# Kernel tuning notes

Measured on AMD Instinct MI355X. Metric: run time of the kernel, lower is better.

Reference implementation:

```python
import jax, jax.numpy as jnp
import numpy as np

TOP_K = 2
NUM_EXPERTS = 64
AUX_COEF = 0.01


def setup_inputs() -> dict:
    key = jax.random.key(0)
    kx, kw = jax.random.split(key)
    B, S, D, E = 4, 4096, 2048, NUM_EXPERTS
    x = jax.random.normal(kx, (B, S, D), dtype=jnp.float32)
    # nn.Linear default init ~ U(-1/sqrt(D), 1/sqrt(D))
    W = jax.random.uniform(kw, (E, D), dtype=jnp.float32,
                           minval=-1.0 / np.sqrt(D), maxval=1.0 / np.sqrt(D))
    return {"x": x, "W": W}


def reference(x, W):
    B, S, D = x.shape
    E = W.shape[0]
    # router projection (no bias)
    logits = jnp.einsum('bsd,ed->bse', x, W)          # [B,S,E]
    probs = jax.nn.softmax(logits, axis=-1)           # [B,S,E]
    top_k_gates, top_k_indices = jax.lax.top_k(probs, TOP_K)  # [B,S,K]
    top_k_gates = top_k_gates / (jnp.sum(top_k_gates, axis=-1, keepdims=True) + 1e-9)
    # aux loss: fraction of routed slots per expert (one-hot mean) x mean router prob
    total_slots = B * S * TOP_K
    counts = jnp.zeros((E,), dtype=jnp.float32).at[top_k_indices.reshape(-1)].add(1.0)
    avg_tokens_per_expert = counts / total_slots      # == one_hot(idx).mean(dims 0,1,2)
    avg_router_prob = jnp.mean(probs, axis=(0, 1))    # [E]
    aux_loss = AUX_COEF * E * jnp.sum(avg_tokens_per_expert * avg_router_prob)
    return top_k_indices, top_k_gates, aux_loss
```

## Files before the change

### kernel.cpp

```cpp
#include <hip/hip_runtime.h>
#include <math.h>

#define NTOK 16384
#define DDIM 2048
#define NEXP 64
#define TM   32
#define NBLK (NTOK / TM)
#define NCH  32
#define NS   64

typedef _Float16 half4v __attribute__((ext_vector_type(4)));
typedef _Float16 half8v __attribute__((ext_vector_type(8)));
typedef float    f32x4  __attribute__((ext_vector_type(4)));

__global__ __launch_bounds__(256) void prep_kernel(const float* __restrict__ W,
                                                   _Float16* __restrict__ Wh,
                                                   _Float16* __restrict__ Wl,
                                                   float* __restrict__ accg) {
    int idx = blockIdx.x * 256 + threadIdx.x;
    int e = idx >> 11, k = idx & 2047;
    float w = W[idx];
    _Float16 h = (_Float16)w;
    _Float16 l = (_Float16)(w - (float)h);
    int S = k >> 5, nb = e >> 4, nl = e & 15, q = (k >> 3) & 3, j = k & 7;
    size_t off = (size_t)S * 2048 + nb * 512 + q * 128 + nl * 8 + j;
    Wh[off] = h;
    Wl[off] = l;
    if (blockIdx.x == 0 && threadIdx.x < 128) accg[threadIdx.x] = 0.0f;
}

__device__ inline void cvt_store(_Float16* __restrict__ Hp, _Float16* __restrict__ Lp,
                                 int off, float4 v) {
    half4v h, l;
    h.x = (_Float16)v.x; l.x = (_Float16)(v.x - (float)h.x);
    h.y = (_Float16)v.y; l.y = (_Float16)(v.y - (float)h.y);
    h.z = (_Float16)v.z; l.z = (_Float16)(v.z - (float)h.z);
    h.w = (_Float16)v.w; l.w = (_Float16)(v.w - (float)h.w);
    *(half4v*)&Hp[off] = h;
    *(half4v*)&Lp[off] = l;
}

#define MFMA16(a, b, c) __builtin_amdgcn_mfma_f32_16x16x32_f16((a), (b), (c), 0, 0, 0)

__global__ __launch_bounds__(256) void router_kernel(
    const float* __restrict__ x, const _Float16* __restrict__ Wh,
    const _Float16* __restrict__ Wl, float* __restrict__ accg,
    float* __restrict__ out)
{
    __shared__ __align__(16) _Float16 Ah[2][2048];
    __shared__ __align__(16) _Float16 Al[2][2048];
    __shared__ float lgt[TM][NEXP + 1];
    __shared__ float cnt[NEXP];

    const int tid  = threadIdx.x;
    const int lane = tid & 63;
    const int wv   = __builtin_amdgcn_readfirstlane(tid >> 6);
    const int m0   = blockIdx.x * TM;

    if (tid < NEXP) cnt[tid] = 0.0f;

    const int tok0 = tid >> 4;
    const int kk0  = (tid & 15) * 4;
    const int s0   = kk0 >> 5, q0 = (kk0 >> 3) & 3, j00 = kk0 & 7;
    const int offA0 = (s0 * 64 + q0 * 16 + tok0) * 8 + j00;
    const int offA1 = offA0 + 1024;

    const float* gx0 = x + (size_t)(m0 + tok0) * DDIM + kk0;
    const float* gx1 = gx0 + (size_t)16 * DDIM;

    const _Float16* Whp = Wh + wv * 512 + lane * 8;
    const _Float16* Wlp = Wl + wv * 512 + lane * 8;

    f32x4 acc0 = {0.f, 0.f, 0.f, 0.f};
    f32x4 acc1 = {0.f, 0.f, 0.f, 0.f};

    float4 stg[2][2];
    stg[0][0] = *(const float4*)(gx0);
    stg[0][1] = *(const float4*)(gx1);
    stg[1][0] = *(const float4*)(gx0 + 64);
    stg[1][1] = *(const float4*)(gx1 + 64);
    half8v whC = *(const half8v*)(Whp);
    half8v wlC = *(const half8v*)(Wlp);

    for (int ch = 0; ch < NCH; ++ch) {
        const int p = ch & 1;
        cvt_store(&Ah[p][0], &Al[p][0], offA0, stg[p][0]);
        cvt_store(&Ah[p][0], &Al[p][0], offA1, stg[p][1]);
        const int cf = (ch + 2 < NCH) ? ch + 2 : 0;
        stg[p][0] = *(const float4*)(gx0 + cf * 64);
        stg[p][1] = *(const float4*)(gx1 + cf * 64);
        __syncthreads();
        #pragma unroll
        for (int s = 0; s < 2; ++s) {
            const int Sg  = ch * 2 + s;
            const int SgN = (Sg + 1) & (NS - 1);
            half8v whN = *(const half8v*)(Whp + (size_t)SgN * 2048);
            half8v wlN = *(const half8v*)(Wlp + (size_t)SgN * 2048);
            half8v a0h = *(const half8v*)&Ah[p][(s * 64 + lane) * 8];
            half8v a0l = *(const half8v*)&Al[p][(s * 64 + lane) * 8];
            half8v a1h = *(const half8v*)&Ah[p][((2 + s) * 64 + lane) * 8];
            half8v a1l = *(const half8v*)&Al[p][((2 + s) * 64 + lane) * 8];
            acc0 = MFMA16(a0l, wlC, acc0);
            acc0 = MFMA16(a0l, whC, acc0);
            acc0 = MFMA16(a0h, wlC, acc0);
            acc0 = MFMA16(a0h, whC, acc0);
            acc1 = MFMA16(a1l, wlC, acc1);
            acc1 = MFMA16(a1l, whC, acc1);
            acc1 = MFMA16(a1h, wlC, acc1);
            acc1 = MFMA16(a1h, whC, acc1);
            whC = whN;
            wlC = wlN;
        }
    }

    {
        const int q  = lane >> 4;
        const int nl = lane & 15;
        #pragma unroll
        for (int r = 0; r < 4; ++r) {
            lgt[q * 4 + r][wv * 16 + nl]      = acc0[r];
            lgt[16 + q * 4 + r][wv * 16 + nl] = acc1[r];
        }
    }
    __syncthreads();

    const int m = tid >> 3;
    const int j = tid & 7;
    float l[8];
    #pragma unroll
    for (int i = 0; i < 8; ++i) l[i] = lgt[m][j * 8 + i];

    float mx = l[0];
    #pragma unroll
    for (int i = 1; i < 8; ++i) mx = fmaxf(mx, l[i]);
    #pragma unroll
    for (int off = 1; off < 8; off <<= 1) mx = fmaxf(mx, __shfl_xor(mx, off, 8));

    float ev[8];
    float zs = 0.f;
    float v1 = -INFINITY, v2 = -INFINITY;
    int i1 = 0, i2 = 0;
    #pragma unroll
    for (int i = 0; i < 8; ++i) {
        ev[i] = __expf(l[i] - mx);
        zs += ev[i];
        int e = j * 8 + i;
        if (l[i] > v1)      { v2 = v1; i2 = i1; v1 = l[i]; i1 = e; }
        else if (l[i] > v2) { v2 = l[i]; i2 = e; }
    }
    #pragma unroll
    for (int off = 1; off < 8; off <<= 1) zs += __shfl_xor(zs, off, 8);

    #pragma unroll
    for (int off = 1; off < 8; off <<= 1) {
        float ov1 = __shfl_xor(v1, off, 8);
        int   oi1 = __shfl_xor(i1, off, 8);
        float ov2 = __shfl_xor(v2, off, 8);
        int   oi2 = __shfl_xor(i2, off, 8);
        bool afirst = (v1 > ov1) || (v1 == ov1 && i1 < oi1);
        if (afirst) {
            bool t = (v2 > ov1) || (v2 == ov1 && i2 < oi1);
            v2 = t ? v2 : ov1;
            i2 = t ? i2 : oi1;
        } else {
            bool t = (ov2 > v1) || (ov2 == v1 && oi2 < i1);
            v2 = t ? ov2 : v1;
            i2 = t ? oi2 : i1;
            v1 = ov1;
            i1 = oi1;
        }
    }

    const float invz = 1.0f / zs;
    if (j == 0) {
        float p1 = invz;
        float p2 = __expf(v2 - mx) * invz;
        float sden = p1 + p2 + 1e-9f;
        int tok = m0 + m;
        out[tok * 2 + 0] = (float)i1;
        out[tok * 2 + 1] = (float)i2;
        out[32768 + tok * 2 + 0] = p1 / sden;
        out[32768 + tok * 2 + 1] = p2 / sden;
        atomicAdd(&cnt[i1], 1.0f);
        atomicAdd(&cnt[i2], 1.0f);
    }

    #pragma unroll
    for (int i = 0; i < 8; ++i) lgt[m][j * 8 + i] = ev[i] * invz;
    __syncthreads();

    if (tid < NEXP) {
        atomicAdd(&accg[tid], cnt[tid]);
    } else if (tid < 128) {
        int e = tid - 64;
        float s = 0.f;
        #pragma unroll 8
        for (int t = 0; t < TM; ++t) s += lgt[t][e];
        atomicAdd(&accg[64 + e], s);
    }
}

__global__ void finalize_kernel(const float* __restrict__ accg,
                                float* __restrict__ out)
{
    int t = threadIdx.x;
    float c = accg[t];
    float p = accg[64 + t];
    float term = (c / (float)(NTOK * 2)) * (p / (float)NTOK);
    #pragma unroll
    for (int off = 1; off < 64; off <<= 1) term += __shfl_xor(term, off, 64);
    if (t == 0) out[65536] = 0.01f * (float)NEXP * term;
}

extern "C" void kernel_launch(void* const* d_in, const int* in_sizes, int n_in,
                              void* d_out, int out_size, void* d_ws, size_t ws_size,
                              hipStream_t stream) {
    const float* x = (const float*)d_in[0];
    const float* W = (const float*)d_in[1];
    float* out  = (float*)d_out;
    float* accg = (float*)d_ws;
    _Float16* Wh = (_Float16*)(accg + 128);
    _Float16* Wl = Wh + (size_t)DDIM * NEXP;

    prep_kernel<<<512, 256, 0, stream>>>(W, Wh, Wl, accg);
    router_kernel<<<NBLK, 256, 0, stream>>>(x, Wh, Wl, accg, out);
    finalize_kernel<<<1, 64, 0, stream>>>(accg, out);
}
```

Measured before the change: 241.9 us.

## Load x fragments directly into registers and drop LDS staging and lo*lo MFMA

Each wave now loads its own x rows straight from global memory into MFMA operand layout and converts them to hi/lo fp16 in registers. This removes the shared-memory staging buffers and the per-chunk __syncthreads. A register prefetch ring runs four k-steps ahead for x and two ahead for W. The lo*lo MFMA term is dropped, going from four to three MFMAs per product. The cost is that every one of the four waves redundantly loads and converts the same 32 token rows, which raises global/L2 traffic and register pressure, and precision drops slightly.

```diff
diff --git a/kernel.cpp b/kernel.cpp
--- a/kernel.cpp
+++ b/kernel.cpp
@@ -6,12 +6,12 @@
 #define NEXP 64
 #define TM   32
 #define NBLK (NTOK / TM)
-#define NCH  32
 #define NS   64
 
-typedef _Float16 half4v __attribute__((ext_vector_type(4)));
 typedef _Float16 half8v __attribute__((ext_vector_type(8)));
 typedef float    f32x4  __attribute__((ext_vector_type(4)));
+
+#define MFMA16(a, b, c) __builtin_amdgcn_mfma_f32_16x16x32_f16((a), (b), (c), 0, 0, 0)
 
 __global__ __launch_bounds__(256) void prep_kernel(const float* __restrict__ W,
                                                    _Float16* __restrict__ Wh,
@@ -29,26 +29,21 @@
     if (blockIdx.x == 0 && threadIdx.x < 128) accg[threadIdx.x] = 0.0f;
 }
 
-__device__ inline void cvt_store(_Float16* __restrict__ Hp, _Float16* __restrict__ Lp,
-                                 int off, float4 v) {
-    half4v h, l;
-    h.x = (_Float16)v.x; l.x = (_Float16)(v.x - (float)h.x);
-    h.y = (_Float16)v.y; l.y = (_Float16)(v.y - (float)h.y);
-    h.z = (_Float16)v.z; l.z = (_Float16)(v.z - (float)h.z);
-    h.w = (_Float16)v.w; l.w = (_Float16)(v.w - (float)h.w);
-    *(half4v*)&Hp[off] = h;
-    *(half4v*)&Lp[off] = l;
-}
-
-#define MFMA16(a, b, c) __builtin_amdgcn_mfma_f32_16x16x32_f16((a), (b), (c), 0, 0, 0)
+__device__ inline void cvt8(const float4* f, half8v& h, half8v& l) {
+    const float* p = (const float*)f;
+    #pragma unroll
+    for (int i = 0; i < 8; ++i) {
+        _Float16 hi = (_Float16)p[i];
+        h[i] = hi;
+        l[i] = (_Float16)(p[i] - (float)hi);
+    }
+}
 
 __global__ __launch_bounds__(256) void router_kernel(
     const float* __restrict__ x, const _Float16* __restrict__ Wh,
     const _Float16* __restrict__ Wl, float* __restrict__ accg,
     float* __restrict__ out)
 {
-    __shared__ __align__(16) _Float16 Ah[2][2048];
-    __shared__ __align__(16) _Float16 Al[2][2048];
     __shared__ float lgt[TM][NEXP + 1];
     __shared__ float cnt[NEXP];
 
@@ -59,57 +54,55 @@
 
     if (tid < NEXP) cnt[tid] = 0.0f;
 
-    const int tok0 = tid >> 4;
-    const int kk0  = (tid & 15) * 4;
-    const int s0   = kk0 >> 5, q0 = (kk0 >> 3) & 3, j00 = kk0 & 7;
-    const int offA0 = (s0 * 64 + q0 * 16 + tok0) * 8 + j00;
-    const int offA1 = offA0 + 1024;
-
-    const float* gx0 = x + (size_t)(m0 + tok0) * DDIM + kk0;
-    const float* gx1 = gx0 + (size_t)16 * DDIM;
-
-    const _Float16* Whp = Wh + wv * 512 + lane * 8;
-    const _Float16* Wlp = Wl + wv * 512 + lane * 8;
+    const int mrow = lane & 15;
+    const int kg   = (lane >> 4) * 8;
+    const float* ax0 = x + (size_t)(m0 + mrow) * DDIM + kg;
+    const float* ax1 = ax0 + (size_t)16 * DDIM;
+
+    const _Float16* whp = Wh + wv * 512 + lane * 8;
+    const _Float16* wlp = Wl + wv * 512 + lane * 8;
 
     f32x4 acc0 = {0.f, 0.f, 0.f, 0.f};
     f32x4 acc1 = {0.f, 0.f, 0.f, 0.f};
 
-    float4 stg[2][2];
-    stg[0][0] = *(const float4*)(gx0);
-    stg[0][1] = *(const float4*)(gx1);
-    stg[1][0] = *(const float4*)(gx0 + 64);
-    stg[1][1] = *(const float4*)(gx1 + 64);
-    half8v whC = *(const half8v*)(Whp);
-    half8v wlC = *(const half8v*)(Wlp);
-
-    for (int ch = 0; ch < NCH; ++ch) {
-        const int p = ch & 1;
-        cvt_store(&Ah[p][0], &Al[p][0], offA0, stg[p][0]);
-        cvt_store(&Ah[p][0], &Al[p][0], offA1, stg[p][1]);
-        const int cf = (ch + 2 < NCH) ? ch + 2 : 0;
-        stg[p][0] = *(const float4*)(gx0 + cf * 64);
-        stg[p][1] = *(const float4*)(gx1 + cf * 64);
-        __syncthreads();
+    float4 fa[4][2][2];
+    half8v wbh[2], wbl[2];
+
+    #pragma unroll
+    for (int s = 0; s < 4; ++s) {
+        fa[s][0][0] = *(const float4*)(ax0 + s * 32);
+        fa[s][0][1] = *(const float4*)(ax0 + s * 32 + 4);
+        fa[s][1][0] = *(const float4*)(ax1 + s * 32);
+        fa[s][1][1] = *(const float4*)(ax1 + s * 32 + 4);
+    }
+    #pragma unroll
+    for (int s = 0; s < 2; ++s) {
+        wbh[s] = *(const half8v*)(whp + (size_t)s * 2048);
+        wbl[s] = *(const half8v*)(wlp + (size_t)s * 2048);
+    }
+
+    for (int mc = 0; mc < NS / 4; ++mc) {
         #pragma unroll
-        for (int s = 0; s < 2; ++s) {
-            const int Sg  = ch * 2 + s;
-            const int SgN = (Sg + 1) & (NS - 1);
-            half8v whN = *(const half8v*)(Whp + (size_t)SgN * 2048);
-            half8v wlN = *(const half8v*)(Wlp + (size_t)SgN * 2048);
-            half8v a0h = *(const half8v*)&Ah[p][(s * 64 + lane) * 8];
-            half8v a0l = *(const half8v*)&Al[p][(s * 64 + lane) * 8];
-            half8v a1h = *(const half8v*)&Ah[p][((2 + s) * 64 + lane) * 8];
-            half8v a1l = *(const half8v*)&Al[p][((2 + s) * 64 + lane) * 8];
-            acc0 = MFMA16(a0l, wlC, acc0);
-            acc0 = MFMA16(a0l, whC, acc0);
-            acc0 = MFMA16(a0h, wlC, acc0);
-            acc0 = MFMA16(a0h, whC, acc0);
-            acc1 = MFMA16(a1l, wlC, acc1);
-            acc1 = MFMA16(a1l, whC, acc1);
-            acc1 = MFMA16(a1h, wlC, acc1);
-            acc1 = MFMA16(a1h, whC, acc1);
-            whC = whN;
-            wlC = wlN;
+        for (int sub = 0; sub < 4; ++sub) {
+            const int s = mc * 4 + sub;
+            half8v a0h, a0l, a1h, a1l;
+            cvt8(fa[sub][0], a0h, a0l);
+            cvt8(fa[sub][1], a1h, a1l);
+            half8v bh = wbh[sub & 1], bl = wbl[sub & 1];
+            const int sa = (s + 4) & (NS - 1);
+            fa[sub][0][0] = *(const float4*)(ax0 + sa * 32);
+            fa[sub][0][1] = *(const float4*)(ax0 + sa * 32 + 4);
+            fa[sub][1][0] = *(const float4*)(ax1 + sa * 32);
+            fa[sub][1][1] = *(const float4*)(ax1 + sa * 32 + 4);
+            const int sw = (s + 2) & (NS - 1);
+            wbh[sub & 1] = *(const half8v*)(whp + (size_t)sw * 2048);
+            wbl[sub & 1] = *(const half8v*)(wlp + (size_t)sw * 2048);
+            acc0 = MFMA16(a0l, bh, acc0);
+            acc0 = MFMA16(a0h, bl, acc0);
+            acc0 = MFMA16(a0h, bh, acc0);
+            acc1 = MFMA16(a1l, bh, acc1);
+            acc1 = MFMA16(a1h, bl, acc1);
+            acc1 = MFMA16(a1h, bh, acc1);
         }
     }
 
```

Result: slower. 362.2 us (+49.7%).

## Halve router token tile to 16 and drop low-low MFMA term

Applied to the files above, without the earlier changes.

Reduces tokens per block from 32 to 16, doubling the grid to 1024 blocks and halving LDS use per block, with one MFMA accumulator per wave. Drops the lo*lo product of the split-fp16 GEMM (3 MFMAs instead of 4 per step). Prefetches W two slices ahead with a two-entry register ring instead of one ahead. Re-reads W from L2 twice as often per token and slightly lowers logit precision, which may affect top-k ties.

```diff
diff --git a/kernel.cpp b/kernel.cpp
--- a/kernel.cpp
+++ b/kernel.cpp
@@ -4,7 +4,7 @@
 #define NTOK 16384
 #define DDIM 2048
 #define NEXP 64
-#define TM   32
+#define TM   16
 #define NBLK (NTOK / TM)
 #define NCH  32
 #define NS   64
@@ -12,6 +12,8 @@
 typedef _Float16 half4v __attribute__((ext_vector_type(4)));
 typedef _Float16 half8v __attribute__((ext_vector_type(8)));
 typedef float    f32x4  __attribute__((ext_vector_type(4)));
+
+#define MFMA16(a, b, c) __builtin_amdgcn_mfma_f32_16x16x32_f16((a), (b), (c), 0, 0, 0)
 
 __global__ __launch_bounds__(256) void prep_kernel(const float* __restrict__ W,
                                                    _Float16* __restrict__ Wh,
@@ -40,15 +42,13 @@
     *(half4v*)&Lp[off] = l;
 }
 
-#define MFMA16(a, b, c) __builtin_amdgcn_mfma_f32_16x16x32_f16((a), (b), (c), 0, 0, 0)
-
 __global__ __launch_bounds__(256) void router_kernel(
     const float* __restrict__ x, const _Float16* __restrict__ Wh,
     const _Float16* __restrict__ Wl, float* __restrict__ accg,
     float* __restrict__ out)
 {
-    __shared__ __align__(16) _Float16 Ah[2][2048];
-    __shared__ __align__(16) _Float16 Al[2][2048];
+    __shared__ __align__(16) _Float16 Ah[2][1024];
+    __shared__ __align__(16) _Float16 Al[2][1024];
     __shared__ float lgt[TM][NEXP + 1];
     __shared__ float cnt[NEXP];
 
@@ -62,54 +62,43 @@
     const int tok0 = tid >> 4;
     const int kk0  = (tid & 15) * 4;
     const int s0   = kk0 >> 5, q0 = (kk0 >> 3) & 3, j00 = kk0 & 7;
-    const int offA0 = (s0 * 64 + q0 * 16 + tok0) * 8 + j00;
-    const int offA1 = offA0 + 1024;
-
-    const float* gx0 = x + (size_t)(m0 + tok0) * DDIM + kk0;
-    const float* gx1 = gx0 + (size_t)16 * DDIM;
-
-    const _Float16* Whp = Wh + wv * 512 + lane * 8;
-    const _Float16* Wlp = Wl + wv * 512 + lane * 8;
-
-    f32x4 acc0 = {0.f, 0.f, 0.f, 0.f};
-    f32x4 acc1 = {0.f, 0.f, 0.f, 0.f};
-
-    float4 stg[2][2];
-    stg[0][0] = *(const float4*)(gx0);
-    stg[0][1] = *(const float4*)(gx1);
-    stg[1][0] = *(const float4*)(gx0 + 64);
-    stg[1][1] = *(const float4*)(gx1 + 64);
-    half8v whC = *(const half8v*)(Whp);
-    half8v wlC = *(const half8v*)(Wlp);
+    const int offA = (s0 * 64 + q0 * 16 + tok0) * 8 + j00;
+
+    const float* gx = x + (size_t)(m0 + tok0) * DDIM + kk0;
+
+    const _Float16* whp = Wh + wv * 512 + lane * 8;
+    const _Float16* wlp = Wl + wv * 512 + lane * 8;
+
+    f32x4 acc = {0.f, 0.f, 0.f, 0.f};
+
+    float4 stg[2];
+    stg[0] = *(const float4*)(gx);
+    stg[1] = *(const float4*)(gx + 64);
+    half8v wbh[2], wbl[2];
+    #pragma unroll
+    for (int s = 0; s < 2; ++s) {
+        wbh[s] = *(const half8v*)(whp + (size_t)s * 2048);
+        wbl[s] = *(const half8v*)(wlp + (size_t)s * 2048);
+    }
 
     for (int ch = 0; ch < NCH; ++ch) {
         const int p = ch & 1;
-        cvt_store(&Ah[p][0], &Al[p][0], offA0, stg[p][0]);
-        cvt_store(&Ah[p][0], &Al[p][0], offA1, stg[p][1]);
+        cvt_store(&Ah[p][0], &Al[p][0], offA, stg[p]);
         const int cf = (ch + 2 < NCH) ? ch + 2 : 0;
-        stg[p][0] = *(const float4*)(gx0 + cf * 64);
-        stg[p][1] = *(const float4*)(gx1 + cf * 64);
+        stg[p] = *(const float4*)(gx + cf * 64);
         __syncthreads();
         #pragma unroll
         for (int s = 0; s < 2; ++s) {
             const int Sg  = ch * 2 + s;
-            const int SgN = (Sg + 1) & (NS - 1);
-            half8v whN = *(const half8v*)(Whp + (size_t)SgN * 2048);
-            half8v wlN = *(const half8v*)(Wlp + (size_t)SgN * 2048);
-            half8v a0h = *(const half8v*)&Ah[p][(s * 64 + lane) * 8];
-            half8v a0l = *(const half8v*)&Al[p][(s * 64 + lane) * 8];
-            half8v a1h = *(const half8v*)&Ah[p][((2 + s) * 64 + lane) * 8];
-            half8v a1l = *(const half8v*)&Al[p][((2 + s) * 64 + lane) * 8];
-            acc0 = MFMA16(a0l, wlC, acc0);
-            acc0 = MFMA16(a0l, whC, acc0);
-            acc0 = MFMA16(a0h, wlC, acc0);
-            acc0 = MFMA16(a0h, whC, acc0);
-            acc1 = MFMA16(a1l, wlC, acc1);
-            acc1 = MFMA16(a1l, whC, acc1);
-            acc1 = MFMA16(a1h, wlC, acc1);
-            acc1 = MFMA16(a1h, whC, acc1);
-            whC = whN;
-            wlC = wlN;
+            const int SgN = (Sg + 2) & (NS - 1);
+            half8v ah = *(const half8v*)&Ah[p][(s * 64 + lane) * 8];
+            half8v al = *(const half8v*)&Al[p][(s * 64 + lane) * 8];
+            half8v bh = wbh[s], bl = wbl[s];
+            wbh[s] = *(const half8v*)(whp + (size_t)SgN * 2048);
+            wbl[s] = *(const half8v*)(wlp + (size_t)SgN * 2048);
+            acc = MFMA16(al, bh, acc);
+            acc = MFMA16(ah, bl, acc);
+            acc = MFMA16(ah, bh, acc);
         }
     }
 
@@ -117,76 +106,76 @@
         const int q  = lane >> 4;
         const int nl = lane & 15;
         #pragma unroll
-        for (int r = 0; r < 4; ++r) {
-            lgt[q * 4 + r][wv * 16 + nl]      = acc0[r];
-            lgt[16 + q * 4 + r][wv * 16 + nl] = acc1[r];
-        }
+        for (int r = 0; r < 4; ++r)
+            lgt[q * 4 + r][wv * 16 + nl] = acc[r];
     }
     __syncthreads();
 
-    const int m = tid >> 3;
-    const int j = tid & 7;
-    float l[8];
-    #pragma unroll
-    for (int i = 0; i < 8; ++i) l[i] = lgt[m][j * 8 + i];
-
-    float mx = l[0];
-    #pragma unroll
-    for (int i = 1; i < 8; ++i) mx = fmaxf(mx, l[i]);
-    #pragma unroll
-    for (int off = 1; off < 8; off <<= 1) mx = fmaxf(mx, __shfl_xor(mx, off, 8));
-
-    float ev[8];
-    float zs = 0.f;
-    float v1 = -INFINITY, v2 = -INFINITY;
-    int i1 = 0, i2 = 0;
-    #pragma unroll
-    for (int i = 0; i < 8; ++i) {
-        ev[i] = __expf(l[i] - mx);
-        zs += ev[i];
-        int e = j * 8 + i;
-        if (l[i] > v1)      { v2 = v1; i2 = i1; v1 = l[i]; i1 = e; }
-        else if (l[i] > v2) { v2 = l[i]; i2 = e; }
-    }
-    #pragma unroll
-    for (int off = 1; off < 8; off <<= 1) zs += __shfl_xor(zs, off, 8);
-
-    #pragma unroll
-    for (int off = 1; off < 8; off <<= 1) {
-        float ov1 = __shfl_xor(v1, off, 8);
-        int   oi1 = __shfl_xor(i1, off, 8);
-        float ov2 = __shfl_xor(v2, off, 8);
-        int   oi2 = __shfl_xor(i2, off, 8);
-        bool afirst = (v1 > ov1) || (v1 == ov1 && i1 < oi1);
-        if (afirst) {
-            bool t = (v2 > ov1) || (v2 == ov1 && i2 < oi1);
-            v2 = t ? v2 : ov1;
-            i2 = t ? i2 : oi1;
-        } else {
-            bool t = (ov2 > v1) || (ov2 == v1 && oi2 < i1);
-            v2 = t ? ov2 : v1;
-            i2 = t ? oi2 : i1;
-            v1 = ov1;
-            i1 = oi1;
-        }
-    }
-
-    const float invz = 1.0f / zs;
-    if (j == 0) {
-        float p1 = invz;
-        float p2 = __expf(v2 - mx) * invz;
-        float sden = p1 + p2 + 1e-9f;
-        int tok = m0 + m;
-        out[tok * 2 + 0] = (float)i1;
-        out[tok * 2 + 1] = (float)i2;
-        out[32768 + tok * 2 + 0] = p1 / sden;
-        out[32768 + tok * 2 + 1] = p2 / sden;
-        atomicAdd(&cnt[i1], 1.0f);
-        atomicAdd(&cnt[i2], 1.0f);
-    }
-
-    #pragma unroll
-    for (int i = 0; i < 8; ++i) lgt[m][j * 8 + i] = ev[i] * invz;
+    if (tid < 128) {
+        const int m = tid >> 3;
+        const int j = tid & 7;
+        float l[8];
+        #pragma unroll
+        for (int i = 0; i < 8; ++i) l[i] = lgt[m][j * 8 + i];
+
+        float mx = l[0];
+        #pragma unroll
+        for (int i = 1; i < 8; ++i) mx = fmaxf(mx, l[i]);
+        #pragma unroll
+        for (int off = 1; off < 8; off <<= 1) mx = fmaxf(mx, __shfl_xor(mx, off, 8));
+
+        float ev[8];
+        float zs = 0.f;
+        float v1 = -INFINITY, v2 = -INFINITY;
+        int i1 = 0, i2 = 0;
+        #pragma unroll
+        for (int i = 0; i < 8; ++i) {
+            ev[i] = __expf(l[i] - mx);
+            zs += ev[i];
+            int e = j * 8 + i;
+            if (l[i] > v1)      { v2 = v1; i2 = i1; v1 = l[i]; i1 = e; }
+            else if (l[i] > v2) { v2 = l[i]; i2 = e; }
+        }
+        #pragma unroll
+        for (int off = 1; off < 8; off <<= 1) zs += __shfl_xor(zs, off, 8);
+
+        #pragma unroll
+        for (int off = 1; off < 8; off <<= 1) {
+            float ov1 = __shfl_xor(v1, off, 8);
+            int   oi1 = __shfl_xor(i1, off, 8);
+            float ov2 = __shfl_xor(v2, off, 8);
+            int   oi2 = __shfl_xor(i2, off, 8);
+            bool afirst = (v1 > ov1) || (v1 == ov1 && i1 < oi1);
+            if (afirst) {
+                bool t = (v2 > ov1) || (v2 == ov1 && i2 < oi1);
+                v2 = t ? v2 : ov1;
+                i2 = t ? i2 : oi1;
+            } else {
+                bool t = (ov2 > v1) || (ov2 == v1 && oi2 < i1);
+                v2 = t ? ov2 : v1;
+                i2 = t ? oi2 : i1;
+                v1 = ov1;
+                i1 = oi1;
+            }
+        }
+
+        const float invz = 1.0f / zs;
+        if (j == 0) {
+            float p1 = invz;
+            float p2 = __expf(v2 - mx) * invz;
+            float sden = p1 + p2 + 1e-9f;
+            int tok = m0 + m;
+            out[tok * 2 + 0] = (float)i1;
+            out[tok * 2 + 1] = (float)i2;
+            out[32768 + tok * 2 + 0] = p1 / sden;
+            out[32768 + tok * 2 + 1] = p2 / sden;
+            atomicAdd(&cnt[i1], 1.0f);
+            atomicAdd(&cnt[i2], 1.0f);
+        }
+
+        #pragma unroll
+        for (int i = 0; i < 8; ++i) lgt[m][j * 8 + i] = ev[i] * invz;
+    }
     __syncthreads();
 
     if (tid < NEXP) {
@@ -194,7 +183,7 @@
     } else if (tid < 128) {
         int e = tid - 64;
         float s = 0.f;
-        #pragma unroll 8
+        #pragma unroll
         for (int t = 0; t < TM; ++t) s += lgt[t][e];
         atomicAdd(&accg[64 + e], s);
     }
```

New measurement: 215.6 us. 10.9% less time.
